# Kernel tuning notes

Measured on AMD Instinct MI355X. Metric: run time of the kernel, lower is better.

Reference implementation:

```python
import jax, jax.numpy as jnp
import numpy as np

B, C, H, W, CLASSES = 128, 30, 15, 15, 16
ROUTINGS = 3
IN_NUM_CAPS = 32 * 11 * 11  # 3872
IN_DIM, OUT_DIM = 8, 16


def squash(x, axis=-1):
    norm = jnp.linalg.norm(x, axis=axis, keepdims=True)
    scale = norm ** 2 / (1 + norm ** 2) / (norm + 1e-8)
    return scale * x


def conv2d(x, w, b):
    y = jax.lax.conv_general_dilated(x, w, (1, 1), 'VALID',
                                     dimension_numbers=('NCHW', 'OIHW', 'NCHW'))
    return y + b[None, :, None, None]


def setup_inputs() -> dict:
    key = jax.random.key(0)
    ks = jax.random.split(key, 12)
    x = jax.random.normal(ks[0], (B, C, H, W), jnp.float32)
    labels = jax.random.randint(ks[1], (B,), 0, CLASSES)
    y = jax.nn.one_hot(labels, CLASSES, dtype=jnp.float32)
    conv1_w = 0.05 * jax.random.normal(ks[2], (256, C, 3, 3), jnp.float32)
    conv1_b = jnp.zeros((256,), jnp.float32)
    bn_gamma = jnp.ones((256,), jnp.float32)
    bn_beta = jnp.zeros((256,), jnp.float32)
    conv2_w = 0.05 * jax.random.normal(ks[3], (256, 256, 3, 3), jnp.float32)
    conv2_b = jnp.zeros((256,), jnp.float32)
    caps_w = 0.01 * jax.random.normal(ks[4], (CLASSES, IN_NUM_CAPS, OUT_DIM, IN_DIM), jnp.float32)
    dec_w1 = 0.05 * jax.random.normal(ks[5], (OUT_DIM * CLASSES, 328), jnp.float32)
    dec_b1 = jnp.zeros((328,), jnp.float32)
    dec_w2 = 0.05 * jax.random.normal(ks[6], (328, 192), jnp.float32)
    dec_b2 = jnp.zeros((192,), jnp.float32)
    dec_w3 = 0.05 * jax.random.normal(ks[7], (192, C * H * W), jnp.float32)
    dec_b3 = jnp.zeros((C * H * W,), jnp.float32)
    return dict(x=x, y=y, conv1_w=conv1_w, conv1_b=conv1_b, bn_gamma=bn_gamma,
                bn_beta=bn_beta, conv2_w=conv2_w, conv2_b=conv2_b, caps_w=caps_w,
                dec_w1=dec_w1, dec_b1=dec_b1, dec_w2=dec_w2, dec_b2=dec_b2,
                dec_w3=dec_w3, dec_b3=dec_b3)


def reference(x, y, conv1_w, conv1_b, bn_gamma, bn_beta, conv2_w, conv2_b,
              caps_w, dec_w1, dec_b1, dec_w2, dec_b2, dec_w3, dec_b3):
    # conv stem: conv -> batchnorm (batch stats, train mode) -> relu
    h = conv2d(x, conv1_w, conv1_b)                        # [B,256,13,13]
    mean = h.mean(axis=(0, 2, 3), keepdims=True)
    var = h.var(axis=(0, 2, 3), keepdims=True)
    h = (h - mean) / jnp.sqrt(var + 1e-5)
    h = h * bn_gamma[None, :, None, None] + bn_beta[None, :, None, None]
    h = jax.nn.relu(h)

    # primary capsules
    p = conv2d(h, conv2_w, conv2_b)                        # [B,256,11,11]
    caps = squash(p.reshape(B, -1, IN_DIM))                # [B,3872,8]

    # dense capsule: prediction vectors + dynamic routing
    x_hat = jnp.einsum('onij,bnj->boni', caps_w, caps)     # [B,16,3872,16]
    x_hat_det = jax.lax.stop_gradient(x_hat)
    b_log = jnp.zeros(x_hat.shape[:3], x_hat.dtype)        # [B,16,3872]
    out = None
    for i in range(ROUTINGS):
        c = jax.nn.softmax(b_log, axis=1)
        xh = x_hat if i == ROUTINGS - 1 else x_hat_det
        out = squash(jnp.einsum('bon,bond->bod', c, xh))   # [B,16,16]
        if i < ROUTINGS - 1:
            b_log = b_log + jnp.einsum('bod,bond->bon', out, x_hat_det)

    length = jnp.linalg.norm(out, axis=-1)                 # [B,16]

    # decoder MLP on label-masked capsules
    masked = (out * y[:, :, None]).reshape(B, -1)          # [B,256]
    r = jax.nn.sigmoid(masked @ dec_w1 + dec_b1)
    r = jax.nn.sigmoid(r @ dec_w2 + dec_b2)
    recon = (r @ dec_w3 + dec_b3).reshape(B, C, H, W)
    return length, recon
```

## Files before the change

kernel.cpp:

```cpp
#include <hip/hip_runtime.h>
#include <hip/hip_bf16.h>

#define NB 128
#define CIN 30
#define HW 15
#define OC 256
#define H1 13
#define H2 11
#define NCAPS 3872
#define IND 8
#define OUTD 16
#define CLS 16
#define D1 328
#define D2 192
#define OUTPIX 6750
#define NSPLIT 242
#define NPB 16
#define RN 2
#define ROUNDS 8

typedef __attribute__((ext_vector_type(8))) short short8_t;
typedef __attribute__((ext_vector_type(4))) float f32x4;
typedef __attribute__((ext_vector_type(4))) unsigned int u32x4;

__device__ inline unsigned bf16rne(float f) {
  unsigned u = __builtin_bit_cast(unsigned, f);
  return (u + 0x7FFF + ((u >> 16) & 1)) >> 16;
}

#define BLO(u) __builtin_bit_cast(float, (unsigned)((u) << 16))
#define BHI(u) __builtin_bit_cast(float, (unsigned)((u) & 0xffff0000u))

__global__ __launch_bounds__(256) void pack_w1_k(const float* __restrict__ w,
    unsigned short* __restrict__ wpk1) {
  int tid = blockIdx.x * blockDim.x + threadIdx.x;
  int j = tid & 7;
  int oc = (tid >> 3) & 255;
  int kc = (tid >> 11) & 3;
  int tap = tid >> 13;
  int ic = kc * 8 + j;
  float v = (ic < CIN) ? w[((size_t)oc * CIN + ic) * 9 + tap] : 0.f;
  wpk1[tid] = (unsigned short)bf16rne(v);
}

__global__ __launch_bounds__(512, 1) void conv1_mfma_k(
    const float* __restrict__ x, const unsigned short* __restrict__ wpk1,
    const float* __restrict__ bias, float* __restrict__ h,
    float* __restrict__ hsum, float* __restrict__ hsum2) {
  __shared__ char smem[128 * 176 * 4];
  unsigned* hs32 = (unsigned*)smem;
  int bid = blockIdx.x;
  int b = bid >> 1;
  int nh = bid & 1;
  int t = threadIdx.x;
  int l = t & 63;
  int wid = t >> 6;

  if (t < 225) {
    const float* xb = x + (size_t)b * (CIN * 225);
#pragma unroll
    for (int icp = 0; icp < 15; icp++) {
      unsigned u0 = bf16rne(xb[(2 * icp) * 225 + t]);
      unsigned u1 = bf16rne(xb[(2 * icp + 1) * 225 + t]);
      hs32[t * 18 + icp] = u0 | (u1 << 16);
    }
    hs32[t * 18 + 15] = 0;
  }
  __syncthreads();

  int row = l & 15, kc = l >> 4;
  int ocb = nh * 128 + wid * 16;

  int arow[11];
#pragma unroll
  for (int mf = 0; mf < 11; mf++) {
    int m = mf * 16 + row;
    int pix = 0;
    if (m < 169) { int oy = m / 13, ox = m - oy * 13; pix = oy * HW + ox; }
    arow[mf] = pix * 72 + kc * 16;
  }

  f32x4 acc[11];
#pragma unroll
  for (int mf = 0; mf < 11; mf++) acc[mf] = (f32x4){0.f, 0.f, 0.f, 0.f};

  const size_t lanebase = ((size_t)ocb + row) * 8;
  const char* lds_base = (const char*)smem;

#pragma unroll
  for (int tap = 0; tap < 9; tap++) {
    const int ky = tap / 3, kx = tap % 3;
    const int koff = (ky * HW + kx) * 72;
    short8_t bfr = *(const short8_t*)(wpk1 + (size_t)(tap * 4 + kc) * 2048 + lanebase);
#pragma unroll
    for (int mf = 0; mf < 11; mf++) {
      short8_t af = *(const short8_t*)(lds_base + arow[mf] + koff);
      acc[mf] = __builtin_amdgcn_mfma_f32_16x16x32_bf16(af, bfr, acc[mf], 0, 0, 0);
    }
  }

  __syncthreads();
  float* cl = (float*)smem;
  {
    int ocl = wid * 16 + row;
#pragma unroll
    for (int mf = 0; mf < 11; mf++) {
      int m0 = mf * 16 + kc * 4;
      *(f32x4*)&cl[ocl * 176 + m0] = acc[mf];
    }
  }
  __syncthreads();
  for (int idx = t; idx < 128 * 169; idx += 512) {
    int ocl = idx / 169;
    int m = idx - ocl * 169;
    int oc = nh * 128 + ocl;
    h[((size_t)b * 256 + oc) * 169 + m] = cl[ocl * 176 + m] + bias[oc];
  }
  {
    int ocl = t >> 2, sub = t & 3;
    float bs = bias[nh * 128 + ocl];
    float s1 = 0.f, s2 = 0.f;
    int m0 = sub * 43, m1 = m0 + 43; if (m1 > 169) m1 = 169;
    for (int m = m0; m < m1; m++) {
      float v = cl[ocl * 176 + m] + bs;
      s1 += v; s2 += v * v;
    }
    s1 += __shfl_xor(s1, 1); s2 += __shfl_xor(s2, 1);
    s1 += __shfl_xor(s1, 2); s2 += __shfl_xor(s2, 2);
    if (sub == 0) {
      hsum[b * 256 + nh * 128 + ocl] = s1;
      hsum2[b * 256 + nh * 128 + ocl] = s2;
    }
  }
}

__global__ __launch_bounds__(128) void bn_finalize_k(const float* __restrict__ hsum,
    const float* __restrict__ hsum2, float* __restrict__ mean, float* __restrict__ istd) {
  int c = blockIdx.x * 128 + threadIdx.x;
  float s = 0.f, s2 = 0.f;
  for (int b = 0; b < NB; b++) {
    s += hsum[b * 256 + c];
    s2 += hsum2[b * 256 + c];
  }
  const float inv_n = 1.0f / (NB * H1 * H1);
  float m = s * inv_n;
  float v = s2 * inv_n - m * m;
  mean[c] = m;
  istd[c] = rsqrtf(v + 1e-5f);
}

__global__ __launch_bounds__(256) void pack_w2_k(const float* __restrict__ w,
    unsigned short* __restrict__ wpk) {
  int tid = blockIdx.x * blockDim.x + threadIdx.x;
  int e = tid & 7;
  int oc = (tid >> 3) & 255;
  int icchunk = (tid >> 11) & 31;
  int kykx = tid >> 16;
  int ic = icchunk * 8 + e;
  wpk[tid] = (unsigned short)bf16rne(w[((size_t)oc * 256 + ic) * 9 + kykx]);
}

__global__ __launch_bounds__(512, 1) void conv2_mfma_k(
    const float* __restrict__ h, const unsigned short* __restrict__ wpk,
    const float* __restrict__ bias, float* __restrict__ p,
    const float* __restrict__ mean, const float* __restrict__ istd,
    const float* __restrict__ gamma, const float* __restrict__ beta) {
  __shared__ char smem[169 * 544];
  unsigned* hs32 = (unsigned*)smem;
  int bid = blockIdx.x;
  int b = bid >> 1;
  int nh = bid & 1;
  int t = threadIdx.x;
  int l = t & 63, wid = t >> 6;

  {
    const float* hb = h + (size_t)b * 256 * 169;
    for (int icp = wid; icp < 128; icp += 8) {
      const float* s0 = hb + (size_t)icp * 2 * 169;
      int c0i = icp * 2, c1i = icp * 2 + 1;
      float a0 = istd[c0i] * gamma[c0i], sh0 = beta[c0i] - mean[c0i] * a0;
      float a1 = istd[c1i] * gamma[c1i], sh1 = beta[c1i] - mean[c1i] * a1;
#pragma unroll
      for (int pb = 0; pb < 3; pb++) {
        int pix = pb * 64 + l;
        if (pix < 169) {
          float v0 = fmaxf(fmaf(s0[pix], a0, sh0), 0.f);
          float v1 = fmaxf(fmaf(s0[169 + pix], a1, sh1), 0.f);
          hs32[pix * 136 + icp] = bf16rne(v0) | (bf16rne(v1) << 16);
        }
      }
    }
  }
  __syncthreads();

  int wm = wid & 1;
  int wn = wid >> 1;
  int row = l & 15, kc = l >> 4;
  int ocb = nh * 128 + wn * 32;

  int abase[4];
#pragma unroll
  for (int mf = 0; mf < 4; mf++) {
    int m = wm * 64 + mf * 16 + row;
    int p0 = (m < 121) ? ((m / 11) * 13 + (m % 11)) : 0;
    abase[mf] = p0 * 544 + kc * 16;
  }

  f32x4 acc[4][2];
#pragma unroll
  for (int mf = 0; mf < 4; mf++)
#pragma unroll
    for (int nf = 0; nf < 2; nf++)
      acc[mf][nf] = (f32x4){0.f, 0.f, 0.f, 0.f};

  const size_t lanebase = ((size_t)kc * 256 + ocb + row) * 8;
  const char* lds_base = (const char*)smem;

  for (int ky = 0; ky < 3; ky++) {
    for (int kx = 0; kx < 3; kx++) {
      int r = ky * 3 + kx;
      int koff = (ky * 13 + kx) * 544;
#pragma unroll
      for (int ks = 0; ks < 8; ks++) {
        short8_t bfr[2];
#pragma unroll
        for (int nf = 0; nf < 2; nf++) {
          size_t idx = lanebase + (size_t)(r * 32 + ks * 4) * 2048 + nf * 128;
          bfr[nf] = *(const short8_t*)(wpk + idx);
        }
        short8_t af[4];
#pragma unroll
        for (int mf = 0; mf < 4; mf++)
          af[mf] = *(const short8_t*)(lds_base + (abase[mf] + koff + ks * 64));
#pragma unroll
        for (int mf = 0; mf < 4; mf++)
#pragma unroll
          for (int nf = 0; nf < 2; nf++)
            acc[mf][nf] = __builtin_amdgcn_mfma_f32_16x16x32_bf16(
                af[mf], bfr[nf], acc[mf][nf], 0, 0, 0);
      }
    }
  }

  __syncthreads();
  float* cl = (float*)smem;
#pragma unroll
  for (int nf = 0; nf < 2; nf++) {
    int ocl = wn * 32 + nf * 16 + row;
#pragma unroll
    for (int mf = 0; mf < 4; mf++) {
      int m0 = wm * 64 + mf * 16 + kc * 4;
      f32x4 v = acc[mf][nf];
      *(f32x4*)&cl[ocl * 132 + m0] = v;
    }
  }
  __syncthreads();
  for (int idx = t; idx < 128 * 128; idx += 512) {
    int ocl = idx >> 7, m = idx & 127;
    if (m < 121) {
      int oc = nh * 128 + ocl;
      p[((size_t)b * 256 + oc) * 121 + m] = cl[ocl * 132 + m] + bias[oc];
    }
  }
}

__global__ __launch_bounds__(256) void squash_caps_k(const float* __restrict__ p,
    float* __restrict__ caps) {
  int tid = blockIdx.x * blockDim.x + threadIdx.x;
  const int total = NB * NCAPS;
  if (tid >= total) return;
  const float4* src = (const float4*)(p + (size_t)tid * 8);
  float4 a = src[0], b4 = src[1];
  float n2 = a.x * a.x + a.y * a.y + a.z * a.z + a.w * a.w +
             b4.x * b4.x + b4.y * b4.y + b4.z * b4.z + b4.w * b4.w;
  float nrm = sqrtf(n2);
  float scale = n2 / (1.0f + n2) / (nrm + 1e-8f);
  a.x *= scale; a.y *= scale; a.z *= scale; a.w *= scale;
  b4.x *= scale; b4.y *= scale; b4.z *= scale; b4.w *= scale;
  float4* dst = (float4*)(caps + (size_t)tid * 8);
  dst[0] = a; dst[1] = b4;
}

__global__ __launch_bounds__(256) void pack_cw_k(const float* __restrict__ cw,
    unsigned short* __restrict__ Wp16) {
  int idx = blockIdx.x * blockDim.x + threadIdx.x;
  int i = idx & 15;
  int j = (idx >> 4) & 7;
  int o = (idx >> 7) & 15;
  int n = idx >> 11;
  Wp16[idx] = (unsigned short)bf16rne(cw[(((size_t)o * NCAPS + n) * 16 + i) * 8 + j]);
}

__global__ __launch_bounds__(256) void route_k(const float* __restrict__ caps,
    const unsigned short* __restrict__ Wp16, const float* __restrict__ osum,
    float* __restrict__ spart0, float* __restrict__ spart1) {
  __shared__ unsigned short wl[2][RN * 2176];
  int id = blockIdx.x;
  int xcd = id & 7;
  int lin = xcd * 121 + (id >> 3);
  int split = lin >> 2;
  int btile = lin & 3;
  int t = threadIdx.x;
  int o = t & 15;
  int bp = t >> 4;
  int b0 = btile * 32 + bp * 2;

  const float* opa = osum + (b0 * 16 + o) * 16;
  f32x4 oa0 = *(const f32x4*)(opa);
  f32x4 oa1 = *(const f32x4*)(opa + 4);
  f32x4 oa2 = *(const f32x4*)(opa + 8);
  f32x4 oa3 = *(const f32x4*)(opa + 12);
  const float* opb = opa + 256;
  f32x4 ob0 = *(const f32x4*)(opb);
  f32x4 ob1 = *(const f32x4*)(opb + 4);
  f32x4 ob2 = *(const f32x4*)(opb + 8);
  f32x4 ob3 = *(const f32x4*)(opb + 12);
  f32x4 sA0 = {0.f,0.f,0.f,0.f}, sA1 = {0.f,0.f,0.f,0.f};
  f32x4 sA2 = {0.f,0.f,0.f,0.f}, sA3 = {0.f,0.f,0.f,0.f};
  f32x4 sB0 = {0.f,0.f,0.f,0.f}, sB1 = {0.f,0.f,0.f,0.f};
  f32x4 sB2 = {0.f,0.f,0.f,0.f}, sB3 = {0.f,0.f,0.f,0.f};

  int nbeg = split * NPB;
  const u32x4* src = (const u32x4*)(Wp16 + (size_t)nbeg * 2048);

  int e0 = t, e1 = t + 256;
  int d0 = (e0 >> 8) * 2176 + ((e0 >> 4) & 15) * 136 + (e0 & 15) * 8;
  int d1 = (e1 >> 8) * 2176 + ((e1 >> 4) & 15) * 136 + (e1 & 15) * 8;

  {
    u32x4 v0 = src[e0], v1 = src[e1];
    *(u32x4*)&wl[0][d0] = v0;
    *(u32x4*)&wl[0][d1] = v1;
  }
  __syncthreads();

  for (int r = 0; r < ROUNDS; r++) {
    u32x4 nv0, nv1;
    if (r < ROUNDS - 1) {
      const u32x4* s2 = src + (r + 1) * 512;
      nv0 = s2[e0]; nv1 = s2[e1];
    }
    const unsigned short* wlb = wl[r & 1];
#pragma unroll
    for (int nl = 0; nl < RN; nl++) {
      int n = nbeg + r * RN + nl;
      const float4* cpa = (const float4*)(caps + ((size_t)b0 * NCAPS + n) * 8);
      const float4* cpb = (const float4*)(caps + ((size_t)(b0 + 1) * NCAPS + n) * 8);
      float4 cqa0 = cpa[0], cqa1 = cpa[1];
      float4 cqb0 = cpb[0], cqb1 = cpb[1];
      float caA[8] = {cqa0.x, cqa0.y, cqa0.z, cqa0.w, cqa1.x, cqa1.y, cqa1.z, cqa1.w};
      float caB[8] = {cqb0.x, cqb0.y, cqb0.z, cqb0.w, cqb1.x, cqb1.y, cqb1.z, cqb1.w};
      const unsigned short* wp = wlb + nl * 2176 + o * 136;
      f32x4 xa0 = {0.f,0.f,0.f,0.f}, xa1 = {0.f,0.f,0.f,0.f};
      f32x4 xa2 = {0.f,0.f,0.f,0.f}, xa3 = {0.f,0.f,0.f,0.f};
      f32x4 xb0 = {0.f,0.f,0.f,0.f}, xb1 = {0.f,0.f,0.f,0.f};
      f32x4 xb2 = {0.f,0.f,0.f,0.f}, xb3 = {0.f,0.f,0.f,0.f};
#pragma unroll
      for (int j = 0; j < 8; j++) {
        u32x4 wA = *(const u32x4*)(wp + j * 16);
        u32x4 wB = *(const u32x4*)(wp + j * 16 + 8);
        f32x4 w0 = {BLO(wA.x), BHI(wA.x), BLO(wA.y), BHI(wA.y)};
        f32x4 w1 = {BLO(wA.z), BHI(wA.z), BLO(wA.w), BHI(wA.w)};
        f32x4 w2 = {BLO(wB.x), BHI(wB.x), BLO(wB.y), BHI(wB.y)};
        f32x4 w3 = {BLO(wB.z), BHI(wB.z), BLO(wB.w), BHI(wB.w)};
        float cjA = caA[j], cjB = caB[j];
        xa0 += w0 * cjA; xa1 += w1 * cjA; xa2 += w2 * cjA; xa3 += w3 * cjA;
        xb0 += w0 * cjB; xb1 += w1 * cjB; xb2 += w2 * cjB; xb3 += w3 * cjB;
      }
      f32x4 pA = oa0 * xa0 + oa1 * xa1 + oa2 * xa2 + oa3 * xa3;
      f32x4 pB = ob0 * xb0 + ob1 * xb1 + ob2 * xb2 + ob3 * xb3;
      float blogA = (pA.x + pA.y) + (pA.z + pA.w);
      float blogB = (pB.x + pB.y) + (pB.z + pB.w);
      float eA = __expf(blogA);
      float eB = __expf(blogB);
      float ssA = eA, ssB = eB;
      ssA += __shfl_xor(ssA, 1); ssB += __shfl_xor(ssB, 1);
      ssA += __shfl_xor(ssA, 2); ssB += __shfl_xor(ssB, 2);
      ssA += __shfl_xor(ssA, 4); ssB += __shfl_xor(ssB, 4);
      ssA += __shfl_xor(ssA, 8); ssB += __shfl_xor(ssB, 8);
      float ccA = eA * __builtin_amdgcn_rcpf(ssA);
      float ccB = eB * __builtin_amdgcn_rcpf(ssB);
      sA0 += xa0 * ccA; sA1 += xa1 * ccA; sA2 += xa2 * ccA; sA3 += xa3 * ccA;
      sB0 += xb0 * ccB; sB1 += xb1 * ccB; sB2 += xb2 * ccB; sB3 += xb3 * ccB;
    }
    if (r < ROUNDS - 1) {
      unsigned short* dst = wl[(r + 1) & 1];
      *(u32x4*)&dst[d0] = nv0;
      *(u32x4*)&dst[d1] = nv1;
      __syncthreads();
    }
  }
  float* base = (split < 121) ? (spart0 + ((size_t)split * NB + b0) * 256)
                              : (spart1 + ((size_t)(split - 121) * NB + b0) * 256);
  float* spA = base + o * 16;
  *(f32x4*)spA = sA0; *(f32x4*)(spA + 4) = sA1;
  *(f32x4*)(spA + 8) = sA2; *(f32x4*)(spA + 12) = sA3;
  float* spB = spA + 256;
  *(f32x4*)spB = sB0; *(f32x4*)(spB + 4) = sB1;
  *(f32x4*)(spB + 8) = sB2; *(f32x4*)(spB + 12) = sB3;
}

__global__ __launch_bounds__(256) void combine_squash_k(const float* __restrict__ spart0,
    const float* __restrict__ spart1, float* __restrict__ osum,
    float* __restrict__ outbuf, const float* __restrict__ y,
    float* __restrict__ masked, float* __restrict__ length_out, int last) {
  int tid = blockIdx.x * blockDim.x + threadIdx.x;
  int i = tid & 15;
  int o = (tid >> 4) & 15;
  int b = tid >> 8;
  float s = 0.f;
  for (int k = 0; k < 121; k++) s += spart0[(size_t)k * 32768 + tid];
  for (int k = 0; k < 121; k++) s += spart1[(size_t)k * 32768 + tid];
  float n2 = s * s;
#pragma unroll
  for (int d = 1; d < 16; d <<= 1) n2 += __shfl_xor(n2, d);
  float nrm = sqrtf(n2);
  float scale = n2 / (1.f + n2) / (nrm + 1e-8f);
  float ov = scale * s;
  outbuf[tid] = ov;
  osum[tid] += ov;
  if (last) {
    masked[tid] = ov * y[b * 16 + o];
    if (i == 0) length_out[b * 16 + o] = scale * nrm;
  }
}

__global__ __launch_bounds__(256) void dec1_k(const float* __restrict__ masked,
    const float* __restrict__ w1, const float* __restrict__ b1, float* __restrict__ r1) {
  int tid = blockIdx.x * blockDim.x + threadIdx.x;
  if (tid >= NB * D1) return;
  int j = tid % D1;
  int b = tid / D1;
  const float* mp = masked + b * 256;
  float acc = b1[j];
  for (int k = 0; k < 256; k++) acc += mp[k] * w1[k * D1 + j];
  r1[tid] = 1.f / (1.f + __expf(-acc));
}

__global__ __launch_bounds__(256) void dec2_k(const float* __restrict__ r1,
    const float* __restrict__ w2, const float* __restrict__ b2, float* __restrict__ r2) {
  int tid = blockIdx.x * blockDim.x + threadIdx.x;
  if (tid >= NB * D2) return;
  int j = tid % D2;
  int b = tid / D2;
  const float* rp = r1 + b * D1;
  float acc = b2[j];
  for (int k = 0; k < D1; k++) acc += rp[k] * w2[k * D2 + j];
  r2[tid] = 1.f / (1.f + __expf(-acc));
}

__global__ __launch_bounds__(256) void dec3_k(const float* __restrict__ r2,
    const float* __restrict__ w3, const float* __restrict__ b3, float* __restrict__ recon) {
  __shared__ float r2s[D2 * 64];
  int mt = blockIdx.x, bh = blockIdx.y;
  int t = threadIdx.x;
  int b0 = bh * 64;
  for (int idx = t; idx < D2 * 64; idx += 256) {
    int bb = idx / D2, k = idx - bb * D2;
    r2s[k * 64 + bb] = r2[(b0 + bb) * D2 + k];
  }
  __syncthreads();
  int moff = t & 63, bg = t >> 6;
  int m = mt * 64 + moff;
  if (m >= OUTPIX) return;
  float acc[16];
#pragma unroll
  for (int q = 0; q < 16; q++) acc[q] = 0.f;
  for (int k = 0; k < D2; k++) {
    float wv = w3[k * OUTPIX + m];
    const float4* r4 = (const float4*)&r2s[k * 64 + bg * 16];
#pragma unroll
    for (int v = 0; v < 4; v++) {
      float4 rv = r4[v];
      acc[v * 4 + 0] += wv * rv.x;
      acc[v * 4 + 1] += wv * rv.y;
      acc[v * 4 + 2] += wv * rv.z;
      acc[v * 4 + 3] += wv * rv.w;
    }
  }
  float bias = b3[m];
#pragma unroll
  for (int q = 0; q < 16; q++) {
    int b = b0 + bg * 16 + q;
    recon[(size_t)b * OUTPIX + m] = acc[q] + bias;
  }
}

extern "C" void kernel_launch(void* const* d_in, const int* in_sizes, int n_in,
                              void* d_out, int out_size, void* d_ws, size_t ws_size,
                              hipStream_t stream) {
  const float* x      = (const float*)d_in[0];
  const float* y      = (const float*)d_in[1];
  const float* conv1w = (const float*)d_in[2];
  const float* conv1b = (const float*)d_in[3];
  const float* gamma  = (const float*)d_in[4];
  const float* beta   = (const float*)d_in[5];
  const float* conv2w = (const float*)d_in[6];
  const float* conv2b = (const float*)d_in[7];
  const float* capsw  = (const float*)d_in[8];
  const float* w1     = (const float*)d_in[9];
  const float* b1     = (const float*)d_in[10];
  const float* w2     = (const float*)d_in[11];
  const float* b2     = (const float*)d_in[12];
  const float* w3     = (const float*)d_in[13];
  const float* b3     = (const float*)d_in[14];

  float* ws = (float*)d_ws;
  float* h      = ws;
  float* p      = h + 5537792;
  float* caps   = p + 3964928;
  float* mean   = caps + 3964928;
  float* istd   = mean + 256;
  float* osum   = istd + 256;
  float* spart0 = osum + 32768;
  float* outb   = spart0 + 3964928;
  float* masked = outb + 32768;
  float* r1     = masked + 32768;
  float* r2     = r1 + 41984;
  unsigned short* wpk = (unsigned short*)(r2 + 24576);
  unsigned short* wpk1 = wpk + 589824;
  unsigned short* Wp16 = (unsigned short*)ws;
  float* spart1 = p;
  float* hsum  = spart0;
  float* hsum2 = spart0 + 32768;

  float* length_out = (float*)d_out;
  float* recon      = (float*)d_out + 2048;

  pack_w1_k<<<73728 / 256, 256, 0, stream>>>(conv1w, wpk1);
  conv1_mfma_k<<<256, 512, 0, stream>>>(x, wpk1, conv1b, h, hsum, hsum2);
  bn_finalize_k<<<2, 128, 0, stream>>>(hsum, hsum2, mean, istd);

  pack_w2_k<<<589824 / 256, 256, 0, stream>>>(conv2w, wpk);
  conv2_mfma_k<<<256, 512, 0, stream>>>(h, wpk, conv2b, p, mean, istd, gamma, beta);

  {
    int total = NB * NCAPS;
    squash_caps_k<<<(total + 255) / 256, 256, 0, stream>>>(p, caps);
  }

  pack_cw_k<<<7929856 / 256, 256, 0, stream>>>(capsw, Wp16);

  hipMemsetAsync(osum, 0, 32768 * sizeof(float), stream);
  for (int it = 0; it < 3; ++it) {
    route_k<<<968, 256, 0, stream>>>(caps, Wp16, osum, spart0, spart1);
    combine_squash_k<<<128, 256, 0, stream>>>(spart0, spart1, osum, outb, y, masked,
                                              length_out, it == 2 ? 1 : 0);
  }

  dec1_k<<<(NB * D1 + 255) / 256, 256, 0, stream>>>(masked, w1, b1, r1);
  dec2_k<<<(NB * D2 + 255) / 256, 256, 0, stream>>>(r1, w2, b2, r2);
  dec3_k<<<dim3((OUTPIX + 63) / 64, 2), 256, 0, stream>>>(r2, w3, b3, recon);
}
```

Measured before the change: 399.2 us.

## Fuse capsule squash into conv2 epilogue and halve routing split count

Result: faster. 363.7 us (-8.9%).

```diff
diff --git a/kernel.cpp b/kernel.cpp
--- a/kernel.cpp
+++ b/kernel.cpp
@@ -14,10 +14,10 @@
 #define D1 328
 #define D2 192
 #define OUTPIX 6750
-#define NSPLIT 242
-#define NPB 16
+#define NSPLIT 121
+#define NPB 32
 #define RN 2
-#define ROUNDS 8
+#define ROUNDS 16
 
 typedef __attribute__((ext_vector_type(8))) short short8_t;
 typedef __attribute__((ext_vector_type(4))) float f32x4;
@@ -162,7 +162,7 @@
 
 __global__ __launch_bounds__(512, 1) void conv2_mfma_k(
     const float* __restrict__ h, const unsigned short* __restrict__ wpk,
-    const float* __restrict__ bias, float* __restrict__ p,
+    const float* __restrict__ bias, float* __restrict__ caps,
     const float* __restrict__ mean, const float* __restrict__ istd,
     const float* __restrict__ gamma, const float* __restrict__ beta) {
   __shared__ char smem[169 * 544];
@@ -255,30 +255,25 @@
     }
   }
   __syncthreads();
-  for (int idx = t; idx < 128 * 128; idx += 512) {
-    int ocl = idx >> 7, m = idx & 127;
-    if (m < 121) {
-      int oc = nh * 128 + ocl;
-      p[((size_t)b * 256 + oc) * 121 + m] = cl[ocl * 132 + m] + bias[oc];
-    }
-  }
-}
-
-__global__ __launch_bounds__(256) void squash_caps_k(const float* __restrict__ p,
-    float* __restrict__ caps) {
-  int tid = blockIdx.x * blockDim.x + threadIdx.x;
-  const int total = NB * NCAPS;
-  if (tid >= total) return;
-  const float4* src = (const float4*)(p + (size_t)tid * 8);
-  float4 a = src[0], b4 = src[1];
-  float n2 = a.x * a.x + a.y * a.y + a.z * a.z + a.w * a.w +
-             b4.x * b4.x + b4.y * b4.y + b4.z * b4.z + b4.w * b4.w;
-  float nrm = sqrtf(n2);
-  float scale = n2 / (1.0f + n2) / (nrm + 1e-8f);
-  a.x *= scale; a.y *= scale; a.z *= scale; a.w *= scale;
-  b4.x *= scale; b4.y *= scale; b4.z *= scale; b4.w *= scale;
-  float4* dst = (float4*)(caps + (size_t)tid * 8);
-  dst[0] = a; dst[1] = b4;
+  for (int g = t; g < 1936; g += 512) {
+    int base = g * 8;
+    float v[8];
+    float n2 = 0.f;
+#pragma unroll
+    for (int e = 0; e < 8; e++) {
+      int idx = base + e;
+      int q = idx / 121, rmd = idx - q * 121;
+      float val = cl[q * 132 + rmd] + bias[nh * 128 + q];
+      v[e] = val;
+      n2 += val * val;
+    }
+    float nrm = sqrtf(n2);
+    float scale = n2 / (1.f + n2) / (nrm + 1e-8f);
+    float4 o0 = {v[0] * scale, v[1] * scale, v[2] * scale, v[3] * scale};
+    float4 o1 = {v[4] * scale, v[5] * scale, v[6] * scale, v[7] * scale};
+    float4* dst = (float4*)(caps + (((size_t)b * NCAPS) + nh * 1936 + g) * 8);
+    dst[0] = o0; dst[1] = o1;
+  }
 }
 
 __global__ __launch_bounds__(256) void pack_cw_k(const float* __restrict__ cw,
@@ -293,11 +288,11 @@
 
 __global__ __launch_bounds__(256) void route_k(const float* __restrict__ caps,
     const unsigned short* __restrict__ Wp16, const float* __restrict__ osum,
-    float* __restrict__ spart0, float* __restrict__ spart1) {
+    float* __restrict__ spart) {
   __shared__ unsigned short wl[2][RN * 2176];
   int id = blockIdx.x;
   int xcd = id & 7;
-  int lin = xcd * 121 + (id >> 3);
+  int lin = (xcd < 4 ? xcd * 61 : 244 + (xcd - 4) * 60) + (id >> 3);
   int split = lin >> 2;
   int btile = lin & 3;
   int t = threadIdx.x;
@@ -390,9 +385,7 @@
       __syncthreads();
     }
   }
-  float* base = (split < 121) ? (spart0 + ((size_t)split * NB + b0) * 256)
-                              : (spart1 + ((size_t)(split - 121) * NB + b0) * 256);
-  float* spA = base + o * 16;
+  float* spA = spart + (((size_t)split * NB + b0) * 16 + o) * 16;
   *(f32x4*)spA = sA0; *(f32x4*)(spA + 4) = sA1;
   *(f32x4*)(spA + 8) = sA2; *(f32x4*)(spA + 12) = sA3;
   float* spB = spA + 256;
@@ -400,17 +393,15 @@
   *(f32x4*)(spB + 8) = sB2; *(f32x4*)(spB + 12) = sB3;
 }
 
-__global__ __launch_bounds__(256) void combine_squash_k(const float* __restrict__ spart0,
-    const float* __restrict__ spart1, float* __restrict__ osum,
-    float* __restrict__ outbuf, const float* __restrict__ y,
+__global__ __launch_bounds__(256) void combine_squash_k(const float* __restrict__ spart,
+    float* __restrict__ osum, float* __restrict__ outbuf, const float* __restrict__ y,
     float* __restrict__ masked, float* __restrict__ length_out, int last) {
   int tid = blockIdx.x * blockDim.x + threadIdx.x;
   int i = tid & 15;
   int o = (tid >> 4) & 15;
   int b = tid >> 8;
   float s = 0.f;
-  for (int k = 0; k < 121; k++) s += spart0[(size_t)k * 32768 + tid];
-  for (int k = 0; k < 121; k++) s += spart1[(size_t)k * 32768 + tid];
+  for (int k = 0; k < NSPLIT; k++) s += spart[(size_t)k * 32768 + tid];
   float n2 = s * s;
 #pragma unroll
   for (int d = 1; d < 16; d <<= 1) n2 += __shfl_xor(n2, d);
@@ -512,17 +503,16 @@
   float* mean   = caps + 3964928;
   float* istd   = mean + 256;
   float* osum   = istd + 256;
-  float* spart0 = osum + 32768;
-  float* outb   = spart0 + 3964928;
+  float* spart  = osum + 32768;
+  float* outb   = spart + 3964928;
   float* masked = outb + 32768;
   float* r1     = masked + 32768;
   float* r2     = r1 + 41984;
   unsigned short* wpk = (unsigned short*)(r2 + 24576);
   unsigned short* wpk1 = wpk + 589824;
   unsigned short* Wp16 = (unsigned short*)ws;
-  float* spart1 = p;
-  float* hsum  = spart0;
-  float* hsum2 = spart0 + 32768;
+  float* hsum  = spart;
+  float* hsum2 = spart + 32768;
 
   float* length_out = (float*)d_out;
   float* recon      = (float*)d_out + 2048;
@@ -532,19 +522,14 @@
   bn_finalize_k<<<2, 128, 0, stream>>>(hsum, hsum2, mean, istd);
 
   pack_w2_k<<<589824 / 256, 256, 0, stream>>>(conv2w, wpk);
-  conv2_mfma_k<<<256, 512, 0, stream>>>(h, wpk, conv2b, p, mean, istd, gamma, beta);
-
-  {
-    int total = NB * NCAPS;
-    squash_caps_k<<<(total + 255) / 256, 256, 0, stream>>>(p, caps);
-  }
+  conv2_mfma_k<<<256, 512, 0, stream>>>(h, wpk, conv2b, caps, mean, istd, gamma, beta);
 
   pack_cw_k<<<7929856 / 256, 256, 0, stream>>>(capsw, Wp16);
 
   hipMemsetAsync(osum, 0, 32768 * sizeof(float), stream);
   for (int it = 0; it < 3; ++it) {
-    route_k<<<968, 256, 0, stream>>>(caps, Wp16, osum, spart0, spart1);
-    combine_squash_k<<<128, 256, 0, stream>>>(spart0, spart1, osum, outb, y, masked,
+    route_k<<<484, 256, 0, stream>>>(caps, Wp16, osum, spart);
+    combine_squash_k<<<128, 256, 0, stream>>>(spart, osum, outb, y, masked,
                                               length_out, it == 2 ? 1 : 0);
   }
 
```
